# Performance work log

Hardware: AMD Instinct MI355X
Metric: run time of the kernel (lower is better)

The kernel has to match this reference:

```python
import jax, jax.numpy as jnp
import numpy as np

N_NODES = 50000
HEADS = 4
OUT_DIM = 64
NEG_SLOPE = 0.2
BETA = 0.5
C_CONST = 1.0
EPS = 1e-16


def setup_inputs() -> dict:
    key = jax.random.key(0)
    ks = jax.random.split(key, 6)
    in_dim = 128
    x = jax.random.normal(ks[0], (N_NODES, in_dim), dtype=jnp.float32)
    edge_index = jax.random.randint(ks[1], (2, 800000), 0, N_NODES, dtype=jnp.int64)
    # GATConv params (glorot-ish scale)
    W = jax.random.normal(ks[2], (in_dim, HEADS * OUT_DIM), dtype=jnp.float32) * (1.0 / np.sqrt(in_dim))
    att_src = jax.random.normal(ks[3], (HEADS, OUT_DIM), dtype=jnp.float32) * (1.0 / np.sqrt(OUT_DIM))
    att_dst = jax.random.normal(ks[4], (HEADS, OUT_DIM), dtype=jnp.float32) * (1.0 / np.sqrt(OUT_DIM))
    bias = jnp.zeros((HEADS * OUT_DIM,), dtype=jnp.float32)
    return {"x": x, "edge_index": edge_index, "W": W, "att_src": att_src,
            "att_dst": att_dst, "bias": bias}


def _gat_conv(x, edge_index, W, att_src, att_dst, bias):
    N = x.shape[0]
    # add self loops (PyG GATConv default)
    loop = jnp.arange(N, dtype=edge_index.dtype)
    src = jnp.concatenate([edge_index[0], loop])
    dst = jnp.concatenate([edge_index[1], loop])
    # linear transform: [N, H, F]
    h = (x @ W).reshape(N, HEADS, OUT_DIM)
    # per-node attention logits: [N, H]
    a_src = jnp.einsum('nhf,hf->nh', h, att_src)
    a_dst = jnp.einsum('nhf,hf->nh', h, att_dst)
    # per-edge logits and segment softmax over destination nodes
    e = jax.nn.leaky_relu(a_src[src] + a_dst[dst], negative_slope=NEG_SLOPE)  # [E, H]
    m = jax.ops.segment_max(e, dst, num_segments=N)                           # [N, H]
    ex = jnp.exp(e - m[dst])
    s = jax.ops.segment_sum(ex, dst, num_segments=N)                          # [N, H]
    alpha = ex / (s[dst] + EPS)                                               # [E, H]
    # aggregate messages: [N, H, F]
    out = jax.ops.segment_sum(alpha[:, :, None] * h[src], dst, num_segments=N)
    return out.reshape(N, HEADS * OUT_DIM) + bias


def reference(x, edge_index, W, att_src, att_dst, bias):
    # eval mode: feature dropout and attention dropout are identity
    z = _gat_conv(x, edge_index, W, att_src, att_dst, bias)
    return BETA * z + (C_CONST - BETA) * jax.nn.elu(z)
```

## Files before the change

kernel.cpp:

```cpp
#include <hip/hip_runtime.h>
#include <hip/hip_bf16.h>

typedef unsigned short u16;
typedef __attribute__((ext_vector_type(8))) short bf16x8;
typedef __attribute__((ext_vector_type(4))) float f32x4;

#define HEADS 4
#define OUT_DIM 64
#define HF 256
#define IN_DIM 128
#define NEG_SLOPE 0.2f
#define EPSF 1e-16f

__device__ __forceinline__ float braw2f(u16 u) {
    union { float f; unsigned int i; } c; c.i = ((unsigned int)u) << 16; return c.f;
}
__device__ __forceinline__ u16 f2braw(float v) {
    __hip_bfloat16 t = __float2bfloat16(v);
    return *(u16*)&t;
}
__device__ __forceinline__ float lrelu(float e) { return e < 0.f ? NEG_SLOPE * e : e; }

__device__ __forceinline__ bool detect_i64(const int* ei) {
    return (ei[1] | ei[3] | ei[5] | ei[7] | ei[9] | ei[11] | ei[13] | ei[15]) == 0;
}
__device__ __forceinline__ void get_edge(const int* ei, int E, int t, bool i64,
                                         int& s, int& d) {
    if (t < E) {
        if (i64) { s = ei[2 * t]; d = ei[2 * (E + t)]; }
        else     { s = ei[t];     d = ei[E + t]; }
    } else {
        s = d = t - E;
    }
}

__global__ __launch_bounds__(256) void init_kernel(const float* __restrict__ W,
                                                   const float* __restrict__ att_s,
                                                   const float* __restrict__ att_d,
                                                   float* __restrict__ wa_s,
                                                   float* __restrict__ wa_d) {
    for (int idx = threadIdx.x; idx < HEADS * IN_DIM; idx += 256) {
        int h = idx >> 7, k = idx & 127;
        float ss = 0.f, sd = 0.f;
        for (int f = 0; f < OUT_DIM; ++f) {
            float wv = W[k * HF + h * OUT_DIM + f];
            ss = fmaf(wv, att_s[h * OUT_DIM + f], ss);
            sd = fmaf(wv, att_d[h * OUT_DIM + f], sd);
        }
        wa_s[idx] = ss;
        wa_d[idx] = sd;
    }
}

__global__ __launch_bounds__(256) void phase1_kernel(const float* __restrict__ x,
                                                     const int* __restrict__ ei,
                                                     const float* __restrict__ W,
                                                     const float* __restrict__ wa_s,
                                                     const float* __restrict__ wa_d,
                                                     float* __restrict__ a_src,
                                                     float* __restrict__ a_dst,
                                                     u16* __restrict__ xb,
                                                     u16* __restrict__ Wfrag,
                                                     int* __restrict__ cnt4,
                                                     int N, int E, int NA, int NC) {
    int b = blockIdx.x;
    if (b < NA) {
        int wid = threadIdx.x >> 6;
        int l = threadIdx.x & 63;
        int g = l >> 4, c = l & 15, kc = c * 8;
        int v = b * 16 + wid * 4 + g;
        if (v >= N) return;

        const float4* xr = (const float4*)(x + (size_t)v * IN_DIM + kc);
        float4 x0 = xr[0], x1 = xr[1];

        uint4 u;
        u.x = (unsigned)f2braw(x0.x) | ((unsigned)f2braw(x0.y) << 16);
        u.y = (unsigned)f2braw(x0.z) | ((unsigned)f2braw(x0.w) << 16);
        u.z = (unsigned)f2braw(x1.x) | ((unsigned)f2braw(x1.y) << 16);
        u.w = (unsigned)f2braw(x1.z) | ((unsigned)f2braw(x1.w) << 16);
        *(uint4*)(xb + (size_t)v * IN_DIM + kc) = u;

        float ps[4], pd[4];
        #pragma unroll
        for (int h = 0; h < 4; ++h) {
            const float4* s4 = (const float4*)(wa_s + h * IN_DIM + kc);
            const float4* d4 = (const float4*)(wa_d + h * IN_DIM + kc);
            float4 s0 = s4[0], s1 = s4[1], d0 = d4[0], d1 = d4[1];
            ps[h] = x0.x*s0.x + x0.y*s0.y + x0.z*s0.z + x0.w*s0.w
                  + x1.x*s1.x + x1.y*s1.y + x1.z*s1.z + x1.w*s1.w;
            pd[h] = x0.x*d0.x + x0.y*d0.y + x0.z*d0.z + x0.w*d0.w
                  + x1.x*d1.x + x1.y*d1.y + x1.z*d1.z + x1.w*d1.w;
        }
        #pragma unroll
        for (int off = 1; off < 16; off <<= 1) {
            #pragma unroll
            for (int h = 0; h < 4; ++h) {
                ps[h] += __shfl_xor(ps[h], off);
                pd[h] += __shfl_xor(pd[h], off);
            }
        }
        if (c == 0) {
            float4 vs, vd;
            vs.x = ps[0]; vs.y = ps[1]; vs.z = ps[2]; vs.w = ps[3];
            vd.x = pd[0]; vd.y = pd[1]; vd.z = pd[2]; vd.w = pd[3];
            *(float4*)(a_src + (size_t)v * HEADS) = vs;
            *(float4*)(a_dst + (size_t)v * HEADS) = vd;
        }
    } else if (b < NA + NC) {
        int t = (b - NA) * 256 + threadIdx.x;
        if (t >= E + N) return;
        bool i64 = detect_i64(ei);
        int src, dst; get_edge(ei, E, t, i64, src, dst);
        if (src >= 0 && src < N && dst >= 0 && dst < N)
            atomicAdd(cnt4 + (t & 3) * N + dst, 1);
    } else {
        int bb = b - NA - NC;
        for (int idx = bb * 256 + threadIdx.x; idx < 32768; idx += 8 * 256) {
            int j = idx & 7, l = (idx >> 3) & 63, t = (idx >> 9) & 3;
            int s = (idx >> 11) & 3, h = (idx >> 13) & 3;
            int k = s * 32 + ((l >> 4) & 3) * 8 + j;
            int col = h * OUT_DIM + t * 16 + (l & 15);
            Wfrag[idx] = f2braw(W[k * HF + col]);
        }
    }
}

__global__ __launch_bounds__(256) void offset_kernel(int* __restrict__ cnt4,
                                                     int* __restrict__ offs,
                                                     int* __restrict__ gcnt,
                                                     int* __restrict__ hist, int N) {
    __shared__ int lh[256];
    lh[threadIdx.x] = 0;
    __syncthreads();

    int idx = blockIdx.x * 256 + threadIdx.x;
    int l = threadIdx.x & 63;
    int d = 0;
    if (idx < N) {
        d = cnt4[idx] + cnt4[N + idx] + cnt4[2 * N + idx] + cnt4[3 * N + idx];
        cnt4[idx] = d;
        atomicAdd(lh + min(max(d, 0), 255), 1);
    }

    int s = d;
    #pragma unroll
    for (int off = 1; off < 64; off <<= 1) {
        int t = __shfl_up(s, off);
        if (l >= off) s += t;
    }
    int base = 0;
    if (l == 63) base = atomicAdd(gcnt, s);
    base = __shfl(base, 63);
    if (idx < N) offs[idx] = base + s - d;

    __syncthreads();
    if (lh[threadIdx.x]) atomicAdd(hist + threadIdx.x, lh[threadIdx.x]);
}

__global__ __launch_bounds__(256) void fillscatter_kernel(const int* __restrict__ ei,
                                                          const int* __restrict__ offs,
                                                          int* __restrict__ cur,
                                                          int* __restrict__ slots,
                                                          uint2* __restrict__ wslots,
                                                          const float* __restrict__ a_src,
                                                          const float* __restrict__ a_dst,
                                                          const int* __restrict__ cnt,
                                                          const int* __restrict__ hist,
                                                          int* __restrict__ bcur,
                                                          int* __restrict__ perm,
                                                          int E, int N, int NC) {
    __shared__ int sc[256];
    __shared__ int lh[256];
    __shared__ int lbase[256];

    int b = blockIdx.x;
    if (b < NC) {
        int t = b * 256 + threadIdx.x;
        if (t >= E + N) return;
        bool i64 = detect_i64(ei);
        int src, dst; get_edge(ei, E, t, i64, src, dst);
        if (src >= 0 && src < N && dst >= 0 && dst < N) {
            int pos = atomicAdd(cur + dst, 1);
            int idx = offs[dst] + pos;
            slots[idx] = src;
            if (wslots) {
                float4 as = ((const float4*)a_src)[src];
                float4 ad = ((const float4*)a_dst)[dst];
                float w0 = __expf(lrelu(as.x + ad.x));
                float w1 = __expf(lrelu(as.y + ad.y));
                float w2 = __expf(lrelu(as.z + ad.z));
                float w3 = __expf(lrelu(as.w + ad.w));
                uint2 wp;
                wp.x = (unsigned)f2braw(w0) | ((unsigned)f2braw(w1) << 16);
                wp.y = (unsigned)f2braw(w2) | ((unsigned)f2braw(w3) << 16);
                wslots[idx] = wp;
            }
        }
    } else {
        int tid = threadIdx.x;
        sc[tid] = hist[tid];
        lh[tid] = 0;
        __syncthreads();
        #pragma unroll
        for (int off = 1; off < 256; off <<= 1) {
            int tv = (tid >= off) ? sc[tid - off] : 0;
            __syncthreads();
            sc[tid] += tv;
            __syncthreads();
        }

        int idx = (b - NC) * 256 + tid;
        int bk = 0, mypos = 0;
        bool valid = (idx < N);
        if (valid) {
            bk = min(max(cnt[idx], 0), 255);
            mypos = atomicAdd(lh + bk, 1);
        }
        __syncthreads();
        int c = lh[tid];
        if (c) lbase[tid] = atomicAdd(bcur + tid, c);
        __syncthreads();
        if (valid) {
            int p = (N - sc[bk]) + lbase[bk] + mypos;
            if (p >= 0 && p < N) perm[p] = idx;
        }
    }
}

#define ACC_EDGE(wp, r) do { \
    float w0_ = braw2f((wp).x & 0xffff), w1_ = braw2f((wp).x >> 16); \
    float w2_ = braw2f((wp).y & 0xffff), w3_ = braw2f((wp).y >> 16); \
    ls0 += w0_; ls1 += w1_; ls2 += w2_; ls3 += w3_; \
    float xv_[8]; \
    xv_[0] = braw2f((r).x & 0xffff); xv_[1] = braw2f((r).x >> 16); \
    xv_[2] = braw2f((r).y & 0xffff); xv_[3] = braw2f((r).y >> 16); \
    xv_[4] = braw2f((r).z & 0xffff); xv_[5] = braw2f((r).z >> 16); \
    xv_[6] = braw2f((r).w & 0xffff); xv_[7] = braw2f((r).w >> 16); \
    _Pragma("unroll") \
    for (int q_ = 0; q_ < 8; ++q_) { \
        G0[q_] = fmaf(w0_, xv_[q_], G0[q_]); \
        G1[q_] = fmaf(w1_, xv_[q_], G1[q_]); \
        G2[q_] = fmaf(w2_, xv_[q_], G2[q_]); \
        G3[q_] = fmaf(w3_, xv_[q_], G3[q_]); \
    } \
} while (0)

__global__ __launch_bounds__(512) void fused_gz_kernel(const int* __restrict__ perm,
                                                       const int* __restrict__ offs,
                                                       const int* __restrict__ cnt,
                                                       const int* __restrict__ slots,
                                                       const uint2* __restrict__ wslots,
                                                       const u16* __restrict__ xb,
                                                       const u16* __restrict__ Wfrag,
                                                       const float* __restrict__ bias,
                                                       float* __restrict__ out,
                                                       int N, int ET) {
    __shared__ u16 smem[32 * 520];
    __shared__ int pvals[32];

    int tid = threadIdx.x;
    int wid = tid >> 6;
    int l = tid & 63;
    int g = l >> 4, c = l & 15, kc = c * 8;
    int n = wid * 4 + g;
    int pidx = blockIdx.x * 32 + n;

    int v = -1;
    if (pidx < N) {
        v = perm[pidx];
        if (v < 0 || v >= N) v = -1;
    }
    if (c == 0) pvals[n] = v;

    int beg = 0, end = 0;
    if (v >= 0) {
        beg = offs[v];
        int deg = cnt[v];
        beg = max(0, min(beg, ET));
        end = max(beg, min(beg + deg, ET));
    }

    float ls0 = 0.f, ls1 = 0.f, ls2 = 0.f, ls3 = 0.f;
    float G0[8] = {0,0,0,0,0,0,0,0};
    float G1[8] = {0,0,0,0,0,0,0,0};
    float G2[8] = {0,0,0,0,0,0,0,0};
    float G3[8] = {0,0,0,0,0,0,0,0};

    int j = beg;
    for (; j + 4 <= end; j += 4) {
        int s0 = max(0, min(slots[j],     N - 1));
        int s1 = max(0, min(slots[j + 1], N - 1));
        int s2 = max(0, min(slots[j + 2], N - 1));
        int s3 = max(0, min(slots[j + 3], N - 1));
        uint2 wp0 = wslots[j];
        uint2 wp1 = wslots[j + 1];
        uint2 wp2 = wslots[j + 2];
        uint2 wp3 = wslots[j + 3];
        uint4 r0 = *(const uint4*)(xb + (size_t)s0 * IN_DIM + kc);
        uint4 r1 = *(const uint4*)(xb + (size_t)s1 * IN_DIM + kc);
        uint4 r2 = *(const uint4*)(xb + (size_t)s2 * IN_DIM + kc);
        uint4 r3 = *(const uint4*)(xb + (size_t)s3 * IN_DIM + kc);
        ACC_EDGE(wp0, r0);
        ACC_EDGE(wp1, r1);
        ACC_EDGE(wp2, r2);
        ACC_EDGE(wp3, r3);
    }
    for (; j < end; ++j) {
        int s0 = max(0, min(slots[j], N - 1));
        uint2 wp0 = wslots[j];
        uint4 r0 = *(const uint4*)(xb + (size_t)s0 * IN_DIM + kc);
        ACC_EDGE(wp0, r0);
    }

    if (v >= 0) {
        float i0 = 1.f / (ls0 + EPSF), i1 = 1.f / (ls1 + EPSF);
        float i2 = 1.f / (ls2 + EPSF), i3 = 1.f / (ls3 + EPSF);
        u16* lp = smem + n * 520 + c * 8;
        #pragma unroll
        for (int h = 0; h < 4; ++h) {
            const float* G = h == 0 ? G0 : h == 1 ? G1 : h == 2 ? G2 : G3;
            float inv = h == 0 ? i0 : h == 1 ? i1 : h == 2 ? i2 : i3;
            uint4 u;
            u.x = (unsigned)f2braw(G[0] * inv) | ((unsigned)f2braw(G[1] * inv) << 16);
            u.y = (unsigned)f2braw(G[2] * inv) | ((unsigned)f2braw(G[3] * inv) << 16);
            u.z = (unsigned)f2braw(G[4] * inv) | ((unsigned)f2braw(G[5] * inv) << 16);
            u.w = (unsigned)f2braw(G[6] * inv) | ((unsigned)f2braw(G[7] * inv) << 16);
            *(uint4*)(lp + h * 128) = u;
        }
    } else {
        u16* lp = smem + n * 520 + c * 8;
        uint4 z = {0, 0, 0, 0};
        #pragma unroll
        for (int h = 0; h < 4; ++h) *(uint4*)(lp + h * 128) = z;
    }
    __syncthreads();

    int t = wid >> 2;
    int h = wid & 3;
    int q = l >> 4, mcol = l & 15;

    const u16* lp = smem + (t * 16 + mcol) * 520 + h * 128 + q * 8;
    bf16x8 A[4];
    A[0] = *(const bf16x8*)(lp);
    A[1] = *(const bf16x8*)(lp + 32);
    A[2] = *(const bf16x8*)(lp + 64);
    A[3] = *(const bf16x8*)(lp + 96);

    f32x4 acc0 = {0.f,0.f,0.f,0.f}, acc1 = acc0, acc2 = acc0, acc3 = acc0;
    #pragma unroll
    for (int s = 0; s < 4; ++s) {
        const u16* wb = Wfrag + (((h * 4 + s) * 4) << 9) + l * 8;
        bf16x8 B0 = *(const bf16x8*)(wb);
        bf16x8 B1 = *(const bf16x8*)(wb + 512);
        bf16x8 B2 = *(const bf16x8*)(wb + 1024);
        bf16x8 B3 = *(const bf16x8*)(wb + 1536);
        acc0 = __builtin_amdgcn_mfma_f32_16x16x32_bf16(A[s], B0, acc0, 0, 0, 0);
        acc1 = __builtin_amdgcn_mfma_f32_16x16x32_bf16(A[s], B1, acc1, 0, 0, 0);
        acc2 = __builtin_amdgcn_mfma_f32_16x16x32_bf16(A[s], B2, acc2, 0, 0, 0);
        acc3 = __builtin_amdgcn_mfma_f32_16x16x32_bf16(A[s], B3, acc3, 0, 0, 0);
    }

    #pragma unroll
    for (int bt = 0; bt < 4; ++bt) {
        f32x4 a = bt == 0 ? acc0 : bt == 1 ? acc1 : bt == 2 ? acc2 : acc3;
        float b = bias[h * OUT_DIM + bt * 16 + mcol];
        #pragma unroll
        for (int r = 0; r < 4; ++r) {
            int vv = pvals[t * 16 + q * 4 + r];
            if (vv >= 0) {
                float z = a[r] + b;
                float y = z > 0.f ? z : 0.5f * z + 0.5f * (__expf(z) - 1.f);
                out[(size_t)vv * HF + h * OUT_DIM + bt * 16 + mcol] = y;
            }
        }
    }
}

__global__ __launch_bounds__(512) void gather_bf_kernel(const int* __restrict__ offs,
                                                        const int* __restrict__ cnt,
                                                        const int* __restrict__ slots,
                                                        const u16* __restrict__ xb,
                                                        const float* __restrict__ a_src,
                                                        const float* __restrict__ a_dst,
                                                        u16* __restrict__ Gout, int N, int ET) {
    int v = (blockIdx.x * 512 + threadIdx.x) >> 6;
    int l = threadIdx.x & 63;
    if (v >= N) return;
    int h = l >> 4, c = l & 15, kc = c * 8;

    int beg = offs[v];
    int deg = cnt[v];
    beg = max(0, min(beg, ET));
    int end = max(beg, min(beg + deg, ET));
    float adh = a_dst[v * HEADS + h];

    float ls = 0.f;
    float G[8] = {0.f,0.f,0.f,0.f,0.f,0.f,0.f,0.f};

    int j = beg;
    for (; j + 4 <= end; j += 4) {
        int s0 = max(0, min(slots[j],     N - 1));
        int s1 = max(0, min(slots[j + 1], N - 1));
        int s2 = max(0, min(slots[j + 2], N - 1));
        int s3 = max(0, min(slots[j + 3], N - 1));
        float w0 = __expf(lrelu(a_src[s0 * HEADS + h] + adh));
        float w1 = __expf(lrelu(a_src[s1 * HEADS + h] + adh));
        float w2 = __expf(lrelu(a_src[s2 * HEADS + h] + adh));
        float w3 = __expf(lrelu(a_src[s3 * HEADS + h] + adh));
        uint4 r0 = *(const uint4*)(xb + (size_t)s0 * IN_DIM + kc);
        uint4 r1 = *(const uint4*)(xb + (size_t)s1 * IN_DIM + kc);
        uint4 r2 = *(const uint4*)(xb + (size_t)s2 * IN_DIM + kc);
        uint4 r3 = *(const uint4*)(xb + (size_t)s3 * IN_DIM + kc);
        ls += (w0 + w1) + (w2 + w3);
        unsigned ua[4];
        ua[0]=r0.x; ua[1]=r0.y; ua[2]=r0.z; ua[3]=r0.w;
        #pragma unroll
        for (int q = 0; q < 4; ++q) {
            G[2*q]   = fmaf(w0, braw2f(ua[q] & 0xffff), G[2*q]);
            G[2*q+1] = fmaf(w0, braw2f(ua[q] >> 16),    G[2*q+1]);
        }
        ua[0]=r1.x; ua[1]=r1.y; ua[2]=r1.z; ua[3]=r1.w;
        #pragma unroll
        for (int q = 0; q < 4; ++q) {
            G[2*q]   = fmaf(w1, braw2f(ua[q] & 0xffff), G[2*q]);
            G[2*q+1] = fmaf(w1, braw2f(ua[q] >> 16),    G[2*q+1]);
        }
        ua[0]=r2.x; ua[1]=r2.y; ua[2]=r2.z; ua[3]=r2.w;
        #pragma unroll
        for (int q = 0; q < 4; ++q) {
            G[2*q]   = fmaf(w2, braw2f(ua[q] & 0xffff), G[2*q]);
            G[2*q+1] = fmaf(w2, braw2f(ua[q] >> 16),    G[2*q+1]);
        }
        ua[0]=r3.x; ua[1]=r3.y; ua[2]=r3.z; ua[3]=r3.w;
        #pragma unroll
        for (int q = 0; q < 4; ++q) {
            G[2*q]   = fmaf(w3, braw2f(ua[q] & 0xffff), G[2*q]);
            G[2*q+1] = fmaf(w3, braw2f(ua[q] >> 16),    G[2*q+1]);
        }
    }
    for (; j < end; ++j) {
        int s0 = max(0, min(slots[j], N - 1));
        float w0 = __expf(lrelu(a_src[s0 * HEADS + h] + adh));
        uint4 r0 = *(const uint4*)(xb + (size_t)s0 * IN_DIM + kc);
        ls += w0;
        unsigned ua[4]; ua[0]=r0.x; ua[1]=r0.y; ua[2]=r0.z; ua[3]=r0.w;
        #pragma unroll
        for (int q = 0; q < 4; ++q) {
            G[2*q]   = fmaf(w0, braw2f(ua[q] & 0xffff), G[2*q]);
            G[2*q+1] = fmaf(w0, braw2f(ua[q] >> 16),    G[2*q+1]);
        }
    }

    float inv = 1.f / (ls + EPSF);
    uint4 u;
    u.x = (unsigned)f2braw(G[0] * inv) | ((unsigned)f2braw(G[1] * inv) << 16);
    u.y = (unsigned)f2braw(G[2] * inv) | ((unsigned)f2braw(G[3] * inv) << 16);
    u.z = (unsigned)f2braw(G[4] * inv) | ((unsigned)f2braw(G[5] * inv) << 16);
    u.w = (unsigned)f2braw(G[6] * inv) | ((unsigned)f2braw(G[7] * inv) << 16);
    *(uint4*)(Gout + (size_t)v * 512 + h * 128 + kc) = u;
}

__global__ __launch_bounds__(512) void gather_f32_kernel(const int* __restrict__ offs,
                                                         const int* __restrict__ cnt,
                                                         const int* __restrict__ slots,
                                                         const float* __restrict__ x,
                                                         const float* __restrict__ a_src,
                                                         const float* __restrict__ a_dst,
                                                         u16* __restrict__ Gout, int N, int ET) {
    int v = (blockIdx.x * 512 + threadIdx.x) >> 6;
    int l = threadIdx.x & 63;
    if (v >= N) return;
    int h = l >> 4, c = l & 15, kc = c * 8;

    int beg = offs[v];
    int deg = cnt[v];
    beg = max(0, min(beg, ET));
    int end = max(beg, min(beg + deg, ET));
    float adh = a_dst[v * HEADS + h];

    float ls = 0.f;
    float G[8] = {0.f,0.f,0.f,0.f,0.f,0.f,0.f,0.f};
    for (int j = beg; j < end; ++j) {
        int s0 = max(0, min(slots[j], N - 1));
        float w0 = __expf(lrelu(a_src[s0 * HEADS + h] + adh));
        const float4* xr0 = (const float4*)(x + (size_t)s0 * IN_DIM + kc);
        float4 a0 = xr0[0], b0 = xr0[1];
        ls += w0;
        G[0]=fmaf(w0,a0.x,G[0]); G[1]=fmaf(w0,a0.y,G[1]);
        G[2]=fmaf(w0,a0.z,G[2]); G[3]=fmaf(w0,a0.w,G[3]);
        G[4]=fmaf(w0,b0.x,G[4]); G[5]=fmaf(w0,b0.y,G[5]);
        G[6]=fmaf(w0,b0.z,G[6]); G[7]=fmaf(w0,b0.w,G[7]);
    }
    float inv = 1.f / (ls + EPSF);
    uint4 u;
    u.x = (unsigned)f2braw(G[0] * inv) | ((unsigned)f2braw(G[1] * inv) << 16);
    u.y = (unsigned)f2braw(G[2] * inv) | ((unsigned)f2braw(G[3] * inv) << 16);
    u.z = (unsigned)f2braw(G[4] * inv) | ((unsigned)f2braw(G[5] * inv) << 16);
    u.w = (unsigned)f2braw(G[6] * inv) | ((unsigned)f2braw(G[7] * inv) << 16);
    *(uint4*)(Gout + (size_t)v * 512 + h * 128 + kc) = u;
}

__global__ __launch_bounds__(256) void zgemm_kernel(const u16* __restrict__ Wfrag,
                                                    const float* __restrict__ bias,
                                                    float* __restrict__ out, int N) {
    int h = threadIdx.x >> 6;
    int l = threadIdx.x & 63;
    int q = l >> 4, mcol = l & 15;
    int nb = blockIdx.x * 16;

    const u16* G = (const u16*)out;
    bool valid = (nb + mcol) < N;
    int vA = valid ? nb + mcol : N - 1;
    const u16* gp = G + (size_t)vA * 512 + h * 128 + q * 8;
    bf16x8 A[4];
    A[0] = *(const bf16x8*)(gp);
    A[1] = *(const bf16x8*)(gp + 32);
    A[2] = *(const bf16x8*)(gp + 64);
    A[3] = *(const bf16x8*)(gp + 96);
    if (!valid) {
        bf16x8 zz = {0,0,0,0,0,0,0,0};
        A[0] = zz; A[1] = zz; A[2] = zz; A[3] = zz;
    }

    f32x4 acc0 = {0.f,0.f,0.f,0.f}, acc1 = acc0, acc2 = acc0, acc3 = acc0;
    #pragma unroll
    for (int s = 0; s < 4; ++s) {
        const u16* wb = Wfrag + (((h * 4 + s) * 4) << 9) + l * 8;
        bf16x8 B0 = *(const bf16x8*)(wb);
        bf16x8 B1 = *(const bf16x8*)(wb + 512);
        bf16x8 B2 = *(const bf16x8*)(wb + 1024);
        bf16x8 B3 = *(const bf16x8*)(wb + 1536);
        acc0 = __builtin_amdgcn_mfma_f32_16x16x32_bf16(A[s], B0, acc0, 0, 0, 0);
        acc1 = __builtin_amdgcn_mfma_f32_16x16x32_bf16(A[s], B1, acc1, 0, 0, 0);
        acc2 = __builtin_amdgcn_mfma_f32_16x16x32_bf16(A[s], B2, acc2, 0, 0, 0);
        acc3 = __builtin_amdgcn_mfma_f32_16x16x32_bf16(A[s], B3, acc3, 0, 0, 0);
    }

    #pragma unroll
    for (int t = 0; t < 4; ++t) {
        f32x4 a = t == 0 ? acc0 : t == 1 ? acc1 : t == 2 ? acc2 : acc3;
        float b = bias[h * OUT_DIM + t * 16 + mcol];
        #pragma unroll
        for (int r = 0; r < 4; ++r) {
            int v = nb + q * 4 + r;
            if (v < N) {
                float z = a[r] + b;
                float y = z > 0.f ? z : 0.5f * z + 0.5f * (__expf(z) - 1.f);
                out[(size_t)v * HF + h * OUT_DIM + t * 16 + mcol] = y;
            }
        }
    }
}

extern "C" void kernel_launch(void* const* d_in, const int* in_sizes, int n_in,
                              void* d_out, int out_size, void* d_ws, size_t ws_size,
                              hipStream_t stream) {
    const float* x       = (const float*)d_in[0];
    const int*   ei      = (const int*)d_in[1];
    const float* W       = (const float*)d_in[2];
    const float* att_src = (const float*)d_in[3];
    const float* att_dst = (const float*)d_in[4];
    const float* bias    = (const float*)d_in[5];

    const int N = in_sizes[0] / IN_DIM;
    const int E = in_sizes[1] / 2;
    const int ET = E + N;
    const int NT = (N + 255) / 256;

    char* ws = (char*)d_ws;
    size_t off = 0;
    float* wa_s   = (float*)(ws + off); off += HEADS * IN_DIM * 4;
    float* wa_d   = (float*)(ws + off); off += HEADS * IN_DIM * 4;
    u16*   Wfrag  = (u16*)(ws + off);   off += 32768 * 2;
    float* a_src  = (float*)(ws + off); off += (size_t)N * HEADS * 4;
    float* a_dst  = (float*)(ws + off); off += (size_t)N * HEADS * 4;
    int*   offs   = (int*)(ws + off);   off += ((size_t)N * 4 + 15) & ~(size_t)15;
    size_t zero_beg = off;
    int*   cnt4   = (int*)(ws + off);   off += ((size_t)N * 16 + 15) & ~(size_t)15;
    int*   cur    = (int*)(ws + off);   off += ((size_t)N * 4 + 15) & ~(size_t)15;
    int*   gcnt   = (int*)(ws + off);   off += 64;
    int*   hist   = (int*)(ws + off);   off += 256 * 4;
    int*   bcur   = (int*)(ws + off);   off += 256 * 4;
    size_t zero_end = off;
    int*   perm   = (int*)(ws + off);   off += ((size_t)N * 4 + 15) & ~(size_t)15;
    int*   slots  = (int*)(ws + off);   off += ((size_t)ET * 4 + 15) & ~(size_t)15;
    u16*   xb     = (u16*)(ws + off);   size_t need_bf = off + (size_t)N * IN_DIM * 2;
    uint2* wslots = (uint2*)(ws + need_bf);
    size_t need_w = need_bf + (size_t)ET * 8;
    bool use_bf = (ws_size >= need_bf);
    bool use_w  = (ws_size >= need_w);

    const int NA = (N + 15) / 16;
    const int NC = (ET + 255) / 256;

    hipMemsetAsync(ws + zero_beg, 0, zero_end - zero_beg, stream);
    init_kernel<<<1, 256, 0, stream>>>(W, att_src, att_dst, wa_s, wa_d);
    phase1_kernel<<<NA + NC + 8, 256, 0, stream>>>(x, ei, W, wa_s, wa_d, a_src, a_dst,
                                                   use_bf ? xb : (u16*)d_out,
                                                   Wfrag, cnt4, N, E, NA, NC);
    offset_kernel<<<NT, 256, 0, stream>>>(cnt4, offs, gcnt, hist, N);
    fillscatter_kernel<<<NC + (use_w ? NT : 0), 256, 0, stream>>>(
        ei, offs, cur, slots, use_w ? wslots : (uint2*)0, a_src, a_dst,
        cnt4, hist, bcur, perm, E, N, NC);
    if (use_w) {
        fused_gz_kernel<<<(N + 31) / 32, 512, 0, stream>>>(perm, offs, cnt4, slots,
                                                           wslots, xb, Wfrag, bias,
                                                           (float*)d_out, N, ET);
    } else if (use_bf) {
        gather_bf_kernel<<<(N * 64 + 511) / 512, 512, 0, stream>>>(offs, cnt4, slots, xb,
                                                                   a_src, a_dst,
                                                                   (u16*)d_out, N, ET);
        zgemm_kernel<<<(N + 15) / 16, 256, 0, stream>>>(Wfrag, bias, (float*)d_out, N);
    } else {
        gather_f32_kernel<<<(N * 64 + 511) / 512, 512, 0, stream>>>(offs, cnt4, slots, x,
                                                                    a_src, a_dst,
                                                                    (u16*)d_out, N, ET);
        zgemm_kernel<<<(N + 15) / 16, 256, 0, stream>>>(Wfrag, bias, (float*)d_out, N);
    }
}
```

Before: 262.6 us.

## Reuse counting-pass atomic positions to place edges without a second atomic pass

The counting pass now records each edge's position returned by its atomicAdd and caches the validated src/dst pair. The offset kernel turns the four sub-counters into per-lane prefix bases. The fill kernel can then compute each edge's CSR slot directly, with no second atomic on a per-destination cursor and no re-decoding of the int64 edge index. This trades extra stores of 12 bytes per edge, plus the matching reads, for the removed atomics, and it only runs when the workspace is large enough.

New measurement: 244.5 us. -6.9%, faster.

```diff
diff --git a/kernel.cpp b/kernel.cpp
--- a/kernel.cpp
+++ b/kernel.cpp
@@ -62,6 +62,8 @@
                                                      u16* __restrict__ xb,
                                                      u16* __restrict__ Wfrag,
                                                      int* __restrict__ cnt4,
+                                                     int* __restrict__ epos,
+                                                     int2* __restrict__ e2,
                                                      int N, int E, int NA, int NC) {
     int b = blockIdx.x;
     if (b < NA) {
@@ -112,8 +114,16 @@
         if (t >= E + N) return;
         bool i64 = detect_i64(ei);
         int src, dst; get_edge(ei, E, t, i64, src, dst);
-        if (src >= 0 && src < N && dst >= 0 && dst < N)
-            atomicAdd(cnt4 + (t & 3) * N + dst, 1);
+        bool ok = (src >= 0 && src < N && dst >= 0 && dst < N);
+        int pos = 0;
+        if (ok) pos = atomicAdd(cnt4 + (t & 3) * N + dst, 1);
+        if (epos) {
+            epos[t] = pos;
+            int2 sd;
+            sd.x = ok ? src : -1;
+            sd.y = ok ? dst : -1;
+            e2[t] = sd;
+        }
     } else {
         int bb = b - NA - NC;
         for (int idx = bb * 256 + threadIdx.x; idx < 32768; idx += 8 * 256) {
@@ -138,8 +148,15 @@
     int l = threadIdx.x & 63;
     int d = 0;
     if (idx < N) {
-        d = cnt4[idx] + cnt4[N + idx] + cnt4[2 * N + idx] + cnt4[3 * N + idx];
+        int c0 = cnt4[idx];
+        int c1 = cnt4[N + idx];
+        int c2 = cnt4[2 * N + idx];
+        int c3 = cnt4[3 * N + idx];
+        d = c0 + c1 + c2 + c3;
         cnt4[idx] = d;
+        cnt4[N + idx] = c0;
+        cnt4[2 * N + idx] = c0 + c1;
+        cnt4[3 * N + idx] = c0 + c1 + c2;
         atomicAdd(lh + min(max(d, 0), 255), 1);
     }
 
@@ -165,10 +182,12 @@
                                                           uint2* __restrict__ wslots,
                                                           const float* __restrict__ a_src,
                                                           const float* __restrict__ a_dst,
-                                                          const int* __restrict__ cnt,
+                                                          const int* __restrict__ cnt4,
                                                           const int* __restrict__ hist,
                                                           int* __restrict__ bcur,
                                                           int* __restrict__ perm,
+                                                          const int* __restrict__ epos,
+                                                          const int2* __restrict__ e2,
                                                           int E, int N, int NC) {
     __shared__ int sc[256];
     __shared__ int lh[256];
@@ -178,24 +197,33 @@
     if (b < NC) {
         int t = b * 256 + threadIdx.x;
         if (t >= E + N) return;
-        bool i64 = detect_i64(ei);
-        int src, dst; get_edge(ei, E, t, i64, src, dst);
-        if (src >= 0 && src < N && dst >= 0 && dst < N) {
+        int src, dst, idx;
+        if (e2) {
+            int2 sd = e2[t];
+            src = sd.x; dst = sd.y;
+            if (src < 0) return;
+            int r = t & 3;
+            int base = (r == 0) ? 0 : cnt4[r * N + dst];
+            idx = offs[dst] + base + epos[t];
+        } else {
+            bool i64 = detect_i64(ei);
+            get_edge(ei, E, t, i64, src, dst);
+            if (!(src >= 0 && src < N && dst >= 0 && dst < N)) return;
             int pos = atomicAdd(cur + dst, 1);
-            int idx = offs[dst] + pos;
-            slots[idx] = src;
-            if (wslots) {
-                float4 as = ((const float4*)a_src)[src];
-                float4 ad = ((const float4*)a_dst)[dst];
-                float w0 = __expf(lrelu(as.x + ad.x));
-                float w1 = __expf(lrelu(as.y + ad.y));
-                float w2 = __expf(lrelu(as.z + ad.z));
-                float w3 = __expf(lrelu(as.w + ad.w));
-                uint2 wp;
-                wp.x = (unsigned)f2braw(w0) | ((unsigned)f2braw(w1) << 16);
-                wp.y = (unsigned)f2braw(w2) | ((unsigned)f2braw(w3) << 16);
-                wslots[idx] = wp;
-            }
+            idx = offs[dst] + pos;
+        }
+        slots[idx] = src;
+        if (wslots) {
+            float4 as = ((const float4*)a_src)[src];
+            float4 ad = ((const float4*)a_dst)[dst];
+            float w0 = __expf(lrelu(as.x + ad.x));
+            float w1 = __expf(lrelu(as.y + ad.y));
+            float w2 = __expf(lrelu(as.z + ad.z));
+            float w3 = __expf(lrelu(as.w + ad.w));
+            uint2 wp;
+            wp.x = (unsigned)f2braw(w0) | ((unsigned)f2braw(w1) << 16);
+            wp.y = (unsigned)f2braw(w2) | ((unsigned)f2braw(w3) << 16);
+            wslots[idx] = wp;
         }
     } else {
         int tid = threadIdx.x;
@@ -214,7 +242,7 @@
         int bk = 0, mypos = 0;
         bool valid = (idx < N);
         if (valid) {
-            bk = min(max(cnt[idx], 0), 255);
+            bk = min(max(cnt4[idx], 0), 255);
             mypos = atomicAdd(lh + bk, 1);
         }
         __syncthreads();
@@ -588,8 +616,13 @@
     u16*   xb     = (u16*)(ws + off);   size_t need_bf = off + (size_t)N * IN_DIM * 2;
     uint2* wslots = (uint2*)(ws + need_bf);
     size_t need_w = need_bf + (size_t)ET * 8;
-    bool use_bf = (ws_size >= need_bf);
-    bool use_w  = (ws_size >= need_w);
+    int*   epos   = (int*)(ws + need_w);
+    int2*  e2     = (int2*)(ws + need_w + ((size_t)ET * 4 + 15 & ~(size_t)15));
+    size_t need_pos = need_w + (((size_t)ET * 4 + 15) & ~(size_t)15)
+                             + (size_t)ET * 8;
+    bool use_bf  = (ws_size >= need_bf);
+    bool use_w   = (ws_size >= need_w);
+    bool use_pos = (ws_size >= need_pos) && use_w;
 
     const int NA = (N + 15) / 16;
     const int NC = (ET + 255) / 256;
@@ -598,11 +631,16 @@
     init_kernel<<<1, 256, 0, stream>>>(W, att_src, att_dst, wa_s, wa_d);
     phase1_kernel<<<NA + NC + 8, 256, 0, stream>>>(x, ei, W, wa_s, wa_d, a_src, a_dst,
                                                    use_bf ? xb : (u16*)d_out,
-                                                   Wfrag, cnt4, N, E, NA, NC);
+                                                   Wfrag, cnt4,
+                                                   use_pos ? epos : (int*)0,
+                                                   use_pos ? e2 : (int2*)0,
+                                                   N, E, NA, NC);
     offset_kernel<<<NT, 256, 0, stream>>>(cnt4, offs, gcnt, hist, N);
     fillscatter_kernel<<<NC + (use_w ? NT : 0), 256, 0, stream>>>(
         ei, offs, cur, slots, use_w ? wslots : (uint2*)0, a_src, a_dst,
-        cnt4, hist, bcur, perm, E, N, NC);
+        cnt4, hist, bcur, perm,
+        use_pos ? epos : (int*)0, use_pos ? e2 : (int2*)0,
+        E, N, NC);
     if (use_w) {
         fused_gz_kernel<<<(N + 31) / 32, 512, 0, stream>>>(perm, offs, cnt4, slots,
                                                            wslots, xb, Wfrag, bias,
```
